# Kernel optimization log

Hardware: AMD Instinct MI355X
Metric: run time of the kernel (lower is better)

## Reference

```python
import jax, jax.numpy as jnp
import numpy as np

D_K = 16
TAU = 1.0


def gumbel_softmax_hard(logits, key, tau=TAU):
    # logits: [B, M]; straight-through hard gumbel-softmax along axis 1
    u = jax.random.uniform(key, logits.shape, minval=1e-10, maxval=1.0)
    g = -jnp.log(-jnp.log(u))
    y_soft = jax.nn.softmax((logits + g) / tau, axis=1)
    idx = jnp.argmax(y_soft, axis=1)
    y_hard = jax.nn.one_hot(idx, logits.shape[1], dtype=logits.dtype)
    return jax.lax.stop_gradient(y_hard - y_soft) + y_soft


def setup_inputs() -> dict:
    key = jax.random.key(0)
    k1, k2, k3, k4 = jax.random.split(key, 4)
    B, NR, NW, DR, DW = 32768, 5, 5, 512, 512
    q = jax.random.normal(k1, (B, NR, DR), dtype=jnp.float32)
    k = jax.random.normal(k2, (B, NW, DW), dtype=jnp.float32)
    # GroupLinearLayer weights: [num_blocks, d_in, d_k], init 0.01*randn (NPS convention)
    w_read = 0.01 * jax.random.normal(k3, (NR, DR, D_K), dtype=jnp.float32)
    w_write = 0.01 * jax.random.normal(k4, (NW, DW, D_K), dtype=jnp.float32)
    return {"q": q, "k": k, "w_read": w_read, "w_write": w_write}


def reference(q, k, w_read, w_write):
    temp = jnp.sqrt(jnp.asarray(D_K, dtype=q.dtype))
    # group-linear (block-diagonal) projections
    read = jnp.einsum('bnd,ndk->bnk', q, w_read)    # [B, NR, d_k]
    write = jnp.einsum('bmd,mdk->bmk', k, w_write)  # [B, NW, d_k]
    # scores for the first two read slots against all write slots
    scores_1 = jnp.einsum('bk,bmk->bm', read[:, 0], write) / temp  # [B, NW]
    scores_2 = jnp.einsum('bk,bmk->bm', read[:, 1], write) / temp  # [B, NW]
    g1 = gumbel_softmax_hard(scores_1, jax.random.key(42))
    g2 = gumbel_softmax_hard(scores_2, jax.random.key(43))
    return (g1, g2)
```

## Files before the change

### kernel.cpp

```cpp
#include <hip/hip_runtime.h>
#include <stdint.h>
#include <math.h>

#define NB    32768
#define NSLOT 5
#define DIM   512
#define DK    16

__device__ __forceinline__ uint32_t rotl32(uint32_t x, uint32_t r) {
  return (x << r) | (x >> (32u - r));
}

__device__ __forceinline__ void threefry2x32_20(uint32_t k0, uint32_t k1,
                                                uint32_t& x0, uint32_t& x1) {
  const uint32_t ks[3] = {k0, k1, k0 ^ k1 ^ 0x1BD11BDAu};
  const uint32_t rotA[4] = {13u, 15u, 26u, 6u};
  const uint32_t rotB[4] = {17u, 29u, 16u, 24u};
  x0 += ks[0];
  x1 += ks[1];
#pragma unroll
  for (int i = 0; i < 5; ++i) {
#pragma unroll
    for (int j = 0; j < 4; ++j) {
      uint32_t r = (i & 1) ? rotB[j] : rotA[j];
      x0 += x1;
      x1 = rotl32(x1, r);
      x1 ^= x0;
    }
    x0 += ks[(i + 1) % 3];
    x1 += ks[(i + 2) % 3] + (uint32_t)(i + 1);
  }
}

__device__ __forceinline__ uint32_t jax_random_bits_part(uint32_t key_lo, uint32_t i) {
  uint32_t x0 = 0u;
  uint32_t x1 = i;
  threefry2x32_20(0u, key_lo, x0, x1);
  return x0 ^ x1;
}

__device__ __forceinline__ float red_dq(float v) {
  v += __shfl_xor(v, 4);
  v += __shfl_xor(v, 8);
  return v;
}

__global__ __launch_bounds__(256) void csa_kernel(
    const float* __restrict__ q,
    const float* __restrict__ kin,
    const float* __restrict__ wr,
    const float* __restrict__ ww,
    float* __restrict__ out)
{
  const int g   = blockIdx.x * 256 + threadIdx.x;
  const int sub = g & 15;
  const int row = g >> 4;
  const int kkq = sub & 3;
  const int dq  = sub >> 2;
  const int dbase = dq * 128;

  float r[2][4];
#pragma unroll
  for (int n = 0; n < 2; ++n) {
    const float4* a4 = (const float4*)(q + ((size_t)row * NSLOT + n) * DIM + dbase);
    const float* wb = wr + (size_t)n * DIM * DK + (size_t)dbase * DK + kkq * 4;
    float ax = 0.f, ay = 0.f, az = 0.f, aw = 0.f;
#pragma unroll 4
    for (int it = 0; it < 32; ++it) {
      float4 av = a4[it];
      float4 w0 = *(const float4*)(wb + (size_t)(it * 4 + 0) * DK);
      float4 w1 = *(const float4*)(wb + (size_t)(it * 4 + 1) * DK);
      float4 w2 = *(const float4*)(wb + (size_t)(it * 4 + 2) * DK);
      float4 w3 = *(const float4*)(wb + (size_t)(it * 4 + 3) * DK);
      ax = fmaf(av.x, w0.x, ax); ay = fmaf(av.x, w0.y, ay);
      az = fmaf(av.x, w0.z, az); aw = fmaf(av.x, w0.w, aw);
      ax = fmaf(av.y, w1.x, ax); ay = fmaf(av.y, w1.y, ay);
      az = fmaf(av.y, w1.z, az); aw = fmaf(av.y, w1.w, aw);
      ax = fmaf(av.z, w2.x, ax); ay = fmaf(av.z, w2.y, ay);
      az = fmaf(av.z, w2.z, az); aw = fmaf(av.z, w2.w, aw);
      ax = fmaf(av.w, w3.x, ax); ay = fmaf(av.w, w3.y, ay);
      az = fmaf(av.w, w3.z, az); aw = fmaf(av.w, w3.w, aw);
    }
    r[n][0] = ax; r[n][1] = ay; r[n][2] = az; r[n][3] = aw;
  }
#pragma unroll
  for (int n = 0; n < 2; ++n)
#pragma unroll
    for (int j = 0; j < 4; ++j) r[n][j] = red_dq(r[n][j]);

  float score[10];
#pragma unroll
  for (int m = 0; m < NSLOT; ++m) {
    const float4* a4 = (const float4*)(kin + ((size_t)row * NSLOT + m) * DIM + dbase);
    const float* wb = ww + (size_t)m * DIM * DK + (size_t)dbase * DK + kkq * 4;
    float ax = 0.f, ay = 0.f, az = 0.f, aw = 0.f;
#pragma unroll 4
    for (int it = 0; it < 32; ++it) {
      float4 av = a4[it];
      float4 w0 = *(const float4*)(wb + (size_t)(it * 4 + 0) * DK);
      float4 w1 = *(const float4*)(wb + (size_t)(it * 4 + 1) * DK);
      float4 w2 = *(const float4*)(wb + (size_t)(it * 4 + 2) * DK);
      float4 w3 = *(const float4*)(wb + (size_t)(it * 4 + 3) * DK);
      ax = fmaf(av.x, w0.x, ax); ay = fmaf(av.x, w0.y, ay);
      az = fmaf(av.x, w0.z, az); aw = fmaf(av.x, w0.w, aw);
      ax = fmaf(av.y, w1.x, ax); ay = fmaf(av.y, w1.y, ay);
      az = fmaf(av.y, w1.z, az); aw = fmaf(av.y, w1.w, aw);
      ax = fmaf(av.z, w2.x, ax); ay = fmaf(av.z, w2.y, ay);
      az = fmaf(av.z, w2.z, az); aw = fmaf(av.z, w2.w, aw);
      ax = fmaf(av.w, w3.x, ax); ay = fmaf(av.w, w3.y, ay);
      az = fmaf(av.w, w3.z, az); aw = fmaf(av.w, w3.w, aw);
    }
    float wc0 = red_dq(ax), wc1 = red_dq(ay), wc2 = red_dq(az), wc3 = red_dq(aw);
    float p0 = r[0][0] * wc0 + r[0][1] * wc1 + r[0][2] * wc2 + r[0][3] * wc3;
    float p1 = r[1][0] * wc0 + r[1][1] * wc1 + r[1][2] * wc2 + r[1][3] * wc3;
    p0 += __shfl_xor(p0, 1); p0 += __shfl_xor(p0, 2);
    p1 += __shfl_xor(p1, 1); p1 += __shfl_xor(p1, 2);
    score[0 * NSLOT + m] = p0 * 0.25f;
    score[1 * NSLOT + m] = p1 * 0.25f;
  }

  if (sub < 2) {
    const int n = sub;
    const uint32_t key_lo = (n == 0) ? 42u : 43u;
    int best = 0;
    float bestv = -INFINITY;
#pragma unroll
    for (int m = 0; m < NSLOT; ++m) {
      uint32_t i = (uint32_t)(row * NSLOT + m);
      uint32_t bits = jax_random_bits_part(key_lo, i);
      float f = __uint_as_float((bits >> 9) | 0x3F800000u) - 1.0f;
      float u = fmaxf(1e-10f, f + 1e-10f);
      double tt = -log((double)u);
      float gmb = (float)(-log(tt));
      float z = score[n * NSLOT + m] + gmb;
      if (z > bestv) { bestv = z; best = m; }
    }
    float* o = out + (size_t)n * (NB * NSLOT) + (size_t)row * NSLOT;
#pragma unroll
    for (int m = 0; m < NSLOT; ++m) o[m] = (m == best) ? 1.0f : 0.0f;
  }
}

extern "C" void kernel_launch(void* const* d_in, const int* in_sizes, int n_in,
                              void* d_out, int out_size, void* d_ws, size_t ws_size,
                              hipStream_t stream) {
  const float* q  = (const float*)d_in[0];
  const float* k  = (const float*)d_in[1];
  const float* wr = (const float*)d_in[2];
  const float* ww = (const float*)d_in[3];
  float* out = (float*)d_out;

  dim3 grid(NB / 16);
  dim3 block(256);
  csa_kernel<<<grid, block, 0, stream>>>(q, k, wr, ww, out);
}
```

Baseline: 842.1 us.

## Stage activation tiles in double-buffered LDS with per-wave DK column split

Restructures the kernel so each 512-thread block handles 64 rows. Each slot/chunk of activations is staged cooperatively into a swizzled, double-buffered shared-memory tile with register prefetch of the next chunk. Each wave then owns two of the 16 projection columns, so weight reads become wave-uniform. Partial scores are reduced across waves through LDS instead of cross-lane shuffles. This aims to improve global load coalescing and overlap loads with compute, at the cost of a block-wide barrier per chunk and a serial tail where only 64 threads do the gumbel/argmax.

```diff
diff --git a/kernel.cpp b/kernel.cpp
--- a/kernel.cpp
+++ b/kernel.cpp
@@ -6,6 +6,14 @@
 #define NSLOT 5
 #define DIM   512
 #define DK    16
+
+#define RPB    64
+#define TPB    512
+#define CH     128
+#define NCHUNK 4
+#define NSL    7
+#define NIT    (NSL * NCHUNK)
+#define ROWSTRIDE (NSLOT * DIM)
 
 __device__ __forceinline__ uint32_t rotl32(uint32_t x, uint32_t r) {
   return (x << r) | (x >> (32u - r));
@@ -39,105 +47,146 @@
   return x0 ^ x1;
 }
 
-__device__ __forceinline__ float red_dq(float v) {
-  v += __shfl_xor(v, 4);
-  v += __shfl_xor(v, 8);
-  return v;
-}
-
-__global__ __launch_bounds__(256) void csa_kernel(
+__global__ __launch_bounds__(TPB) void csa_kernel(
     const float* __restrict__ q,
     const float* __restrict__ kin,
     const float* __restrict__ wr,
     const float* __restrict__ ww,
     float* __restrict__ out)
 {
-  const int g   = blockIdx.x * 256 + threadIdx.x;
-  const int sub = g & 15;
-  const int row = g >> 4;
-  const int kkq = sub & 3;
-  const int dq  = sub >> 2;
-  const int dbase = dq * 128;
-
-  float r[2][4];
-#pragma unroll
-  for (int n = 0; n < 2; ++n) {
-    const float4* a4 = (const float4*)(q + ((size_t)row * NSLOT + n) * DIM + dbase);
-    const float* wb = wr + (size_t)n * DIM * DK + (size_t)dbase * DK + kkq * 4;
-    float ax = 0.f, ay = 0.f, az = 0.f, aw = 0.f;
-#pragma unroll 4
-    for (int it = 0; it < 32; ++it) {
-      float4 av = a4[it];
-      float4 w0 = *(const float4*)(wb + (size_t)(it * 4 + 0) * DK);
-      float4 w1 = *(const float4*)(wb + (size_t)(it * 4 + 1) * DK);
-      float4 w2 = *(const float4*)(wb + (size_t)(it * 4 + 2) * DK);
-      float4 w3 = *(const float4*)(wb + (size_t)(it * 4 + 3) * DK);
-      ax = fmaf(av.x, w0.x, ax); ay = fmaf(av.x, w0.y, ay);
-      az = fmaf(av.x, w0.z, az); aw = fmaf(av.x, w0.w, aw);
-      ax = fmaf(av.y, w1.x, ax); ay = fmaf(av.y, w1.y, ay);
-      az = fmaf(av.y, w1.z, az); aw = fmaf(av.y, w1.w, aw);
-      ax = fmaf(av.z, w2.x, ax); ay = fmaf(av.z, w2.y, ay);
-      az = fmaf(av.z, w2.z, az); aw = fmaf(av.z, w2.w, aw);
-      ax = fmaf(av.w, w3.x, ax); ay = fmaf(av.w, w3.y, ay);
-      az = fmaf(av.w, w3.z, az); aw = fmaf(av.w, w3.w, aw);
-    }
-    r[n][0] = ax; r[n][1] = ay; r[n][2] = az; r[n][3] = aw;
-  }
-#pragma unroll
-  for (int n = 0; n < 2; ++n)
-#pragma unroll
-    for (int j = 0; j < 4; ++j) r[n][j] = red_dq(r[n][j]);
-
-  float score[10];
-#pragma unroll
-  for (int m = 0; m < NSLOT; ++m) {
-    const float4* a4 = (const float4*)(kin + ((size_t)row * NSLOT + m) * DIM + dbase);
-    const float* wb = ww + (size_t)m * DIM * DK + (size_t)dbase * DK + kkq * 4;
-    float ax = 0.f, ay = 0.f, az = 0.f, aw = 0.f;
-#pragma unroll 4
-    for (int it = 0; it < 32; ++it) {
-      float4 av = a4[it];
-      float4 w0 = *(const float4*)(wb + (size_t)(it * 4 + 0) * DK);
-      float4 w1 = *(const float4*)(wb + (size_t)(it * 4 + 1) * DK);
-      float4 w2 = *(const float4*)(wb + (size_t)(it * 4 + 2) * DK);
-      float4 w3 = *(const float4*)(wb + (size_t)(it * 4 + 3) * DK);
-      ax = fmaf(av.x, w0.x, ax); ay = fmaf(av.x, w0.y, ay);
-      az = fmaf(av.x, w0.z, az); aw = fmaf(av.x, w0.w, aw);
-      ax = fmaf(av.y, w1.x, ax); ay = fmaf(av.y, w1.y, ay);
-      az = fmaf(av.y, w1.z, az); aw = fmaf(av.y, w1.w, aw);
-      ax = fmaf(av.z, w2.x, ax); ay = fmaf(av.z, w2.y, ay);
-      az = fmaf(av.z, w2.z, az); aw = fmaf(av.z, w2.w, aw);
-      ax = fmaf(av.w, w3.x, ax); ay = fmaf(av.w, w3.y, ay);
-      az = fmaf(av.w, w3.z, az); aw = fmaf(av.w, w3.w, aw);
-    }
-    float wc0 = red_dq(ax), wc1 = red_dq(ay), wc2 = red_dq(az), wc3 = red_dq(aw);
-    float p0 = r[0][0] * wc0 + r[0][1] * wc1 + r[0][2] * wc2 + r[0][3] * wc3;
-    float p1 = r[1][0] * wc0 + r[1][1] * wc1 + r[1][2] * wc2 + r[1][3] * wc3;
-    p0 += __shfl_xor(p0, 1); p0 += __shfl_xor(p0, 2);
-    p1 += __shfl_xor(p1, 1); p1 += __shfl_xor(p1, 2);
-    score[0 * NSLOT + m] = p0 * 0.25f;
-    score[1 * NSLOT + m] = p1 * 0.25f;
-  }
-
-  if (sub < 2) {
-    const int n = sub;
-    const uint32_t key_lo = (n == 0) ? 42u : 43u;
-    int best = 0;
-    float bestv = -INFINITY;
-#pragma unroll
-    for (int m = 0; m < NSLOT; ++m) {
-      uint32_t i = (uint32_t)(row * NSLOT + m);
-      uint32_t bits = jax_random_bits_part(key_lo, i);
-      float f = __uint_as_float((bits >> 9) | 0x3F800000u) - 1.0f;
-      float u = fmaxf(1e-10f, f + 1e-10f);
-      double tt = -log((double)u);
-      float gmb = (float)(-log(tt));
-      float z = score[n * NSLOT + m] + gmb;
-      if (z > bestv) { bestv = z; best = m; }
-    }
-    float* o = out + (size_t)n * (NB * NSLOT) + (size_t)row * NSLOT;
-#pragma unroll
-    for (int m = 0; m < NSLOT; ++m) o[m] = (m == best) ? 1.0f : 0.0f;
+  __shared__ __align__(16) float buf[2][RPB * CH];
+
+  const int t      = threadIdx.x;
+  const int lane   = t & 63;
+  const int kg     = __builtin_amdgcn_readfirstlane(t >> 6);
+  const int c0     = kg * 2;
+  const int r7     = lane & 7;
+  const int row_g0 = blockIdx.x * RPB;
+
+  const int t5  = t >> 5;
+  const int d4s = t & 31;
+
+  float rcomp[2][2];
+  float pscr[10];
+  float acc0 = 0.f, acc1 = 0.f;
+
+  auto aslot = [&](int s) -> const float* {
+    return (s < 2) ? (q + (size_t)row_g0 * ROWSTRIDE + s * DIM)
+                   : (kin + (size_t)row_g0 * ROWSTRIDE + (s - 2) * DIM);
+  };
+
+  float4 sreg[4];
+
+  {
+    const float* ab = aslot(0);
+#pragma unroll
+    for (int jj = 0; jj < 4; ++jj) {
+      int sr = jj * 16 + t5;
+      sreg[jj] = *(const float4*)(ab + (size_t)sr * ROWSTRIDE + d4s * 4);
+    }
+#pragma unroll
+    for (int jj = 0; jj < 4; ++jj) {
+      int sr = jj * 16 + t5;
+      *(float4*)(&buf[0][sr * CH + ((d4s ^ (sr & 7)) << 2)]) = sreg[jj];
+    }
+  }
+  __syncthreads();
+
+#pragma unroll 1
+  for (int it = 0; it < NIT; ++it) {
+    const int s   = it >> 2;
+    const int c   = it & 3;
+    const int nit = it + 1;
+
+    if (nit < NIT) {
+      const int ns = nit >> 2, nc = nit & 3;
+      const float* ab = aslot(ns) + nc * CH;
+#pragma unroll
+      for (int jj = 0; jj < 4; ++jj) {
+        int sr = jj * 16 + t5;
+        sreg[jj] = *(const float4*)(ab + (size_t)sr * ROWSTRIDE + d4s * 4);
+      }
+    }
+
+    {
+      const float* wsl = (s < 2) ? (wr + s * (DIM * DK)) : (ww + (s - 2) * (DIM * DK));
+      const float* wp  = wsl + c * (CH * DK) + c0;
+      const float* bp  = &buf[it & 1][lane * CH];
+#pragma unroll
+      for (int d4 = 0; d4 < 32; ++d4) {
+        const float4 av = *(const float4*)(bp + ((d4 ^ r7) << 2));
+        const float* wd = wp + d4 * 4 * DK;
+        float2 w0 = *(const float2*)(wd + 0 * DK);
+        float2 w1 = *(const float2*)(wd + 1 * DK);
+        float2 w2 = *(const float2*)(wd + 2 * DK);
+        float2 w3 = *(const float2*)(wd + 3 * DK);
+        acc0 = fmaf(av.x, w0.x, acc0); acc1 = fmaf(av.x, w0.y, acc1);
+        acc0 = fmaf(av.y, w1.x, acc0); acc1 = fmaf(av.y, w1.y, acc1);
+        acc0 = fmaf(av.z, w2.x, acc0); acc1 = fmaf(av.z, w2.y, acc1);
+        acc0 = fmaf(av.w, w3.x, acc0); acc1 = fmaf(av.w, w3.y, acc1);
+      }
+    }
+
+    if (c == 3) {
+      if (s < 2) {
+        rcomp[s][0] = acc0; rcomp[s][1] = acc1;
+      } else {
+        const int m = s - 2;
+        pscr[0 * NSLOT + m] = rcomp[0][0] * acc0 + rcomp[0][1] * acc1;
+        pscr[1 * NSLOT + m] = rcomp[1][0] * acc0 + rcomp[1][1] * acc1;
+      }
+      acc0 = 0.f; acc1 = 0.f;
+    }
+
+    if (nit < NIT) {
+      float* bd = &buf[nit & 1][0];
+#pragma unroll
+      for (int jj = 0; jj < 4; ++jj) {
+        int sr = jj * 16 + t5;
+        *(float4*)(bd + sr * CH + ((d4s ^ (sr & 7)) << 2)) = sreg[jj];
+      }
+    }
+    __syncthreads();
+  }
+
+  float* psc = &buf[0][0];
+  {
+    float* pd = psc + (kg * RPB + lane) * 10;
+#pragma unroll
+    for (int j = 0; j < 10; ++j) pd[j] = pscr[j];
+  }
+  __syncthreads();
+
+  if (t < RPB) {
+    const int row_g = row_g0 + t;
+    float sc[10];
+#pragma unroll
+    for (int j = 0; j < 10; ++j) {
+      float sum = 0.f;
+#pragma unroll
+      for (int g = 0; g < 8; ++g) sum += psc[(g * RPB + t) * 10 + j];
+      sc[j] = sum * 0.25f;
+    }
+#pragma unroll
+    for (int n = 0; n < 2; ++n) {
+      const uint32_t key_lo = (n == 0) ? 42u : 43u;
+      int best = 0;
+      float bestv = -INFINITY;
+#pragma unroll
+      for (int m = 0; m < NSLOT; ++m) {
+        uint32_t i = (uint32_t)(row_g * NSLOT + m);
+        uint32_t bits = jax_random_bits_part(key_lo, i);
+        float f = __uint_as_float((bits >> 9) | 0x3F800000u) - 1.0f;
+        float u = fmaxf(1e-10f, f + 1e-10f);
+        double tt = -log((double)u);
+        float gmb = (float)(-log(tt));
+        float z = sc[n * NSLOT + m] + gmb;
+        if (z > bestv) { bestv = z; best = m; }
+      }
+      float* o = out + (size_t)n * (NB * NSLOT) + (size_t)row_g * NSLOT;
+#pragma unroll
+      for (int m = 0; m < NSLOT; ++m) o[m] = (m == best) ? 1.0f : 0.0f;
+    }
   }
 }
 
@@ -150,7 +199,7 @@
   const float* ww = (const float*)d_in[3];
   float* out = (float*)d_out;
 
-  dim3 grid(NB / 16);
-  dim3 block(256);
+  dim3 grid(NB / RPB);
+  dim3 block(TPB);
   csa_kernel<<<grid, block, 0, stream>>>(q, k, wr, ww, out);
 }
```

Result: slower. 906.9 us (+7.7%).
